# Kernel optimization log

Measured on AMD Instinct MI355X. Metric: run time of the kernel, lower is better.

## Reference

```python
import jax, jax.numpy as jnp
import numpy as np

C, FF, NH = 128, 2048, 8
B, D, H, W = 1, 16, 16, 16
EPS = 1e-5

def setup_inputs() -> dict:
    key = jax.random.key(0)
    ks = jax.random.split(key, 20)
    s = 0.02
    inp = {
        'x': jax.random.normal(ks[0], (B, C, D, H, W), jnp.float32),
        'Wq': jax.random.normal(ks[1], (C, C), jnp.float32) * s,
        'bq': jnp.zeros((C,), jnp.float32),
        'Wk': jax.random.normal(ks[2], (C, C), jnp.float32) * s,
        'bk': jnp.zeros((C,), jnp.float32),
        'Wv': jax.random.normal(ks[3], (C, C), jnp.float32) * s,
        'bv': jnp.zeros((C,), jnp.float32),
        'Wo': jax.random.normal(ks[4], (C, C), jnp.float32) * s,
        'bo': jnp.zeros((C,), jnp.float32),
        'W1': jax.random.normal(ks[5], (FF, C), jnp.float32) * s,
        'b1': jnp.zeros((FF,), jnp.float32),
        'W2': jax.random.normal(ks[6], (C, FF), jnp.float32) * s,
        'b2': jnp.zeros((C,), jnp.float32),
        'g1': jnp.ones((C,), jnp.float32),
        'be1': jnp.zeros((C,), jnp.float32),
        'g2': jnp.ones((C,), jnp.float32),
        'be2': jnp.zeros((C,), jnp.float32),
    }
    return inp

def _layernorm(t, g, b):
    # normalize over last (channel) dim, biased variance like torch LayerNorm
    m = jnp.mean(t, axis=-1, keepdims=True)
    v = jnp.mean(jnp.square(t - m), axis=-1, keepdims=True)
    return (t - m) * jax.lax.rsqrt(v + EPS) * g + b

def reference(x, Wq, bq, Wk, bk, Wv, bv, Wo, bo, W1, b1, W2, b2, g1, be1, g2, be2):
    b_, c, d, h, w = x.shape
    n = d * h * w
    hd = c // NH
    xf = x.reshape(b_, c, n)  # [B,C,N]
    # 1x1 conv3d == per-voxel linear over channels
    q = jnp.einsum('oc,bcn->bon', Wq, xf) + bq[:, None]
    k = jnp.einsum('oc,bcn->bon', Wk, xf) + bk[:, None]
    v = jnp.einsum('oc,bcn->bon', Wv, xf) + bv[:, None]
    q = q.reshape(b_, NH, hd, n)
    k = k.reshape(b_, NH, hd, n)
    v = v.reshape(b_, NH, hd, n)
    scores = jnp.einsum('bhcd,bhce->bhde', q, k) / (hd ** 0.5)  # [B,NH,N,N]
    probs = jax.nn.softmax(scores, axis=-1)
    attn = jnp.einsum('bhde,bhce->bhcd', probs, v).reshape(b_, c, n)
    attn = jnp.einsum('oc,bcn->bon', Wo, attn) + bo[:, None]
    x1 = xf + attn  # residual (dropout = identity at eval)
    x1 = _layernorm(x1.transpose(0, 2, 1), g1, be1)  # [B,N,C]
    hmid = jax.nn.relu(jnp.einsum('fc,bnc->bnf', W1, x1) + b1)
    ffn = jnp.einsum('cf,bnf->bnc', W2, hmid) + b2
    x2 = _layernorm(x1 + ffn, g2, be2)
    return x2.transpose(0, 2, 1).reshape(b_, c, d, h, w)
```

## Files before the change

### kernel.cpp

```cpp
#include <hip/hip_runtime.h>
#include <hip/hip_bf16.h>

typedef __hip_bfloat16 bf16;
typedef short short8 __attribute__((ext_vector_type(8)));
typedef float f32x4 __attribute__((ext_vector_type(4)));

#define C_   128
#define N_   4096
#define NH_  8
#define HD_  16
#define FF_  2048
#define SCALE_Q 0.360673760222241f

__device__ __forceinline__ unsigned short f2bf_bits(float f) {
    bf16 h = __float2bfloat16(f);
    return *reinterpret_cast<unsigned short*>(&h);
}
__device__ __forceinline__ unsigned int pack_trunc(float lo, float hi) {
    return (__float_as_uint(hi) & 0xffff0000u) | (__float_as_uint(lo) >> 16);
}
__device__ __forceinline__ short f2bf_trunc(float f) {
    return (short)(__float_as_uint(f) >> 16);
}
__device__ __forceinline__ float bfs2f(short s) {
    return __uint_as_float(((unsigned int)(unsigned short)s) << 16);
}
__device__ __forceinline__ float fast_exp2(float x) {
    return __builtin_amdgcn_exp2f(x);
}
__device__ __forceinline__ f32x4 mfma16(short8 a, short8 b, f32x4 c) {
    return __builtin_amdgcn_mfma_f32_16x16x32_bf16(a, b, c, 0, 0, 0);
}
__device__ __forceinline__ int kpos(int ko) { return ((ko & 15) << 1) + (ko >> 4); }

__global__ void k_prep(const float* __restrict__ Wq, const float* __restrict__ Wk,
                       const float* __restrict__ Wv, const float* __restrict__ Wo,
                       const float* __restrict__ W1, const float* __restrict__ W2,
                       const float* __restrict__ x,
                       bf16* __restrict__ Wqkvf, bf16* __restrict__ Wof,
                       bf16* __restrict__ W1f, bf16* __restrict__ W2f,
                       bf16* __restrict__ xTf)
{
    const int i = blockIdx.x * 256 + threadIdx.x;
    if (i < 49152) {
        const int o = i >> 7, k = i & 127;
        const float v = (o < 128) ? Wq[i] : (o < 256) ? Wk[i - 16384] : Wv[i - 32768];
        const int pk = kpos(k & 31);
        Wqkvf[(((o >> 4) << 2) + (k >> 5)) * 512 + (((pk >> 3) << 4) + (o & 15)) * 8 + (pk & 7)]
            = __float2bfloat16(v);
    } else if (i < 65536) {
        const int j = i - 49152, o = j >> 7, k = j & 127;
        const int pk = kpos(k & 31);
        Wof[(((o >> 4) << 2) + (k >> 5)) * 512 + (((pk >> 3) << 4) + (o & 15)) * 8 + (pk & 7)]
            = __float2bfloat16(Wo[j]);
    } else if (i < 327680) {
        const int j = i - 65536, o = j >> 7, k = j & 127;
        const int pk = kpos(k & 31);
        W1f[(((o >> 4) << 2) + (k >> 5)) * 512 + (((pk >> 3) << 4) + (o & 15)) * 8 + (pk & 7)]
            = __float2bfloat16(W1[j]);
    } else if (i < 589824) {
        const int j = i - 327680, o = j >> 11, k = j & 2047;
        const int pk = kpos(k & 31);
        W2f[(((o >> 4) << 6) + (k >> 5)) * 512 + (((pk >> 3) << 4) + (o & 15)) * 8 + (pk & 7)]
            = __float2bfloat16(W2[j]);
    } else if (i < 1114112) {
        const int j = i - 589824, c = j >> 12, n = j & 4095;
        const int pk = kpos(c & 31);
        xTf[(((n >> 4) << 2) + (c >> 5)) * 512 + (((pk >> 3) << 4) + (n & 15)) * 8 + (pk & 7)]
            = __float2bfloat16(x[j]);
    }
}

__global__ void __launch_bounds__(256) k_qkv(
    const bf16* __restrict__ xTf, const bf16* __restrict__ Wqkvf,
    const float* __restrict__ bq, const float* __restrict__ bk, const float* __restrict__ bv,
    bf16* __restrict__ qf, bf16* __restrict__ kf, bf16* __restrict__ vf)
{
    const int tid = threadIdx.x, wave = tid >> 6, lane = tid & 63;
    const int col = lane & 15, quad = lane >> 4;
    const int gw = blockIdx.x * 4 + wave;
    const int rt = gw / 24, ct = gw % 24;
    f32x4 acc = {};
    #pragma unroll
    for (int c = 0; c < 4; ++c) {
        short8 a = *(const short8*)(xTf + ((size_t)(rt * 4 + c) << 9) + lane * 8);
        short8 b = *(const short8*)(Wqkvf + ((size_t)(ct * 4 + c) << 9) + lane * 8);
        acc = mfma16(a, b, acc);
    }
    #pragma unroll
    for (int r = 0; r < 4; ++r) {
        const int m = rt * 16 + quad * 4 + r;
        const int n = ct * 16 + col;
        const float v = acc[r];
        if (n < 128) {
            const int h = n >> 4, ch = n & 15;
            qf[((h << 8) + (m >> 4)) * 256 + (((ch >> 3) << 4) + (m & 15)) * 8 + (ch & 7)] =
                __float2bfloat16((v + bq[n]) * SCALE_Q);
        } else if (n < 256) {
            const int c2 = n - 128, h = c2 >> 4, ch = c2 & 15;
            kf[((h << 8) + (m >> 4)) * 256 + (((ch >> 3) << 4) + (m & 15)) * 8 + (ch & 7)] =
                __float2bfloat16(v + bk[c2]);
        } else {
            const int c2 = n - 256, h = c2 >> 4, ch = c2 & 15;
            const int ko = m & 31;
            const int pos = ((ko & 15) << 1) + (ko >> 4);
            vf[((h << 7) + (m >> 5)) * 512 + (((pos >> 3) << 4) + ch) * 8 + (pos & 7)] =
                __float2bfloat16(v + bv[c2]);
        }
    }
}

__global__ void __launch_bounds__(256)
attn_kernel(const bf16* __restrict__ qf, const bf16* __restrict__ kf,
            const bf16* __restrict__ vf, bf16* __restrict__ af)
{
    __shared__ __align__(16) union {
        unsigned int P[4][2][320];
        float comb[4][64][8];
    } sh;
    const int tid = threadIdx.x, wave = tid >> 6, lane = tid & 63;
    const int col = lane & 15, quad = lane >> 4;
    const int gw = blockIdx.x;
    const int h  = gw >> 8;
    const int tile = gw & 255;
    const f32x4 zero = {};

    short8 aq = {};
    if (quad < 2)
        aq = *(const short8*)(qf + ((size_t)((h << 8) + tile) << 8) + lane * 8);

    f32x4 accO0 = {}, accO1 = {};
    float L[4] = {0.f, 0.f, 0.f, 0.f};

    const int kbeg = wave << 10;
    unsigned int* P0 = &sh.P[wave][0][0];
    unsigned int* P1 = &sh.P[wave][1][0];

    for (int i = 0; i < 32; i += 2) {
        const int mA = kbeg + (i << 5);
        const int mB = mA + 32;

        short8 bkA0 = {}, bkA1 = {}, bkB0 = {}, bkB1 = {};
        if (quad < 2) {
            const bf16* ka = kf + ((size_t)((h << 8) + (mA >> 4)) << 8) + lane * 8;
            bkA0 = *(const short8*)(ka);
            bkA1 = *(const short8*)(ka + 256);
            bkB0 = *(const short8*)(ka + 512);
            bkB1 = *(const short8*)(ka + 768);
        }
        f32x4 s0 = mfma16(aq, bkA0, zero);
        f32x4 s1 = mfma16(aq, bkA1, zero);
        f32x4 s2 = mfma16(aq, bkB0, zero);
        f32x4 s3 = mfma16(aq, bkB1, zero);
        #pragma unroll
        for (int r = 0; r < 4; ++r) {
            const float p0 = fast_exp2(s0[r]);
            const float p1 = fast_exp2(s1[r]);
            const float p2 = fast_exp2(s2[r]);
            const float p3 = fast_exp2(s3[r]);
            L[r] += (p0 + p1) + (p2 + p3);
            P0[(quad * 4 + r) * 20 + col] = pack_trunc(p0, p1);
            P1[(quad * 4 + r) * 20 + col] = pack_trunc(p2, p3);
        }
        short8 vA = *(const short8*)(vf + ((size_t)((h << 7) + (mA >> 5)) << 9) + lane * 8);
        short8 vB = *(const short8*)(vf + ((size_t)((h << 7) + (mB >> 5)) << 9) + lane * 8);
        short8 ap0 = *(const short8*)((const short*)P0 + col * 40 + quad * 8);
        accO0 = mfma16(ap0, vA, accO0);
        short8 ap1 = *(const short8*)((const short*)P1 + col * 40 + quad * 8);
        accO1 = mfma16(ap1, vB, accO1);
    }

    f32x4 accO;
    #pragma unroll
    for (int r = 0; r < 4; ++r) accO[r] = accO0[r] + accO1[r];

    __syncthreads();
    #pragma unroll
    for (int r = 0; r < 4; ++r) {
        sh.comb[wave][lane][r]     = accO[r];
        sh.comb[wave][lane][4 + r] = L[r];
    }
    __syncthreads();

    if (wave == 0) {
        #pragma unroll
        for (int r = 0; r < 4; ++r) {
            float O = sh.comb[0][lane][r] + sh.comb[1][lane][r]
                    + sh.comb[2][lane][r] + sh.comb[3][lane][r];
            float l = sh.comb[0][lane][4+r] + sh.comb[1][lane][4+r]
                    + sh.comb[2][lane][4+r] + sh.comb[3][lane][4+r];
            l += __shfl_xor(l, 1); l += __shfl_xor(l, 2);
            l += __shfl_xor(l, 4); l += __shfl_xor(l, 8);
            const int row16 = quad * 4 + r;
            const int pk = (col << 1) + (h & 1);
            af[((tile << 2) + (h >> 1)) * 512 + (((pk >> 3) << 4) + row16) * 8 + (pk & 7)] =
                __float2bfloat16(O / l);
        }
    }
}

__global__ void __launch_bounds__(256, 1)
k_mega(const bf16* __restrict__ af, const bf16* __restrict__ xTf,
       const bf16* __restrict__ Wof, const bf16* __restrict__ W1f, const bf16* __restrict__ W2f,
       const float* __restrict__ bo, const float* __restrict__ b1, const float* __restrict__ b2,
       const float* __restrict__ g1, const float* __restrict__ be1,
       const float* __restrict__ g2, const float* __restrict__ be2,
       float* __restrict__ out)
{
    __shared__ __align__(16) unsigned int Pb[4][2][320];
    __shared__ float comb[96][64];
    const int tid = threadIdx.x, wave = tid >> 6, lane = tid & 63;
    const int col = lane & 15, quad = lane >> 4;
    const int rt = blockIdx.x, n0 = rt << 4;
    const f32x4 zero = {};

    short8 ao[4], xt[4];
    #pragma unroll
    for (int c = 0; c < 4; ++c) {
        ao[c] = *(const short8*)(af  + ((size_t)(rt * 4 + c) << 9) + lane * 8);
        xt[c] = *(const short8*)(xTf + ((size_t)(rt * 4 + c) << 9) + lane * 8);
    }
    f32x4 d[8];
    #pragma unroll
    for (int t = 0; t < 8; ++t) d[t] = zero;
    #pragma unroll
    for (int t = 0; t < 8; ++t)
        #pragma unroll
        for (int c = 0; c < 4; ++c) {
            short8 b = *(const short8*)(Wof + ((size_t)(t * 4 + c) << 9) + lane * 8);
            d[t] = mfma16(ao[c], b, d[t]);
        }
    #pragma unroll
    for (int t = 0; t < 8; ++t) {
        const float bt = bo[t * 16 + col];
        #pragma unroll
        for (int r = 0; r < 4; ++r) d[t][r] += bt;
    }

    float x1f[4][8];
    #pragma unroll
    for (int c = 0; c < 4; ++c) {
        unsigned int* Pw = &Pb[wave][c & 1][0];
        const short* Ps = (const short*)Pw;
        #pragma unroll
        for (int r = 0; r < 4; ++r)
            Pw[(quad * 4 + r) * 20 + col] = pack_trunc(d[2 * c][r], d[2 * c + 1][r]);
        short8 ar = *(const short8*)(Ps + col * 40 + quad * 8);
        #pragma unroll
        for (int j = 0; j < 8; ++j)
            x1f[c][j] = bfs2f(ar[j]) + bfs2f(xt[c][j]);
    }

    float s = 0.f, ss = 0.f;
    #pragma unroll
    for (int c = 0; c < 4; ++c)
        #pragma unroll
        for (int j = 0; j < 8; ++j) { s += x1f[c][j]; ss += x1f[c][j] * x1f[c][j]; }
    s  += __shfl_xor(s, 16);  s  += __shfl_xor(s, 32);
    ss += __shfl_xor(ss, 16); ss += __shfl_xor(ss, 32);
    const float m1 = s * (1.f / 128.f);
    const float rstd1 = rsqrtf(ss * (1.f / 128.f) - m1 * m1 + 1e-5f);
    short8 aq1[4];
    #pragma unroll
    for (int c = 0; c < 4; ++c)
        #pragma unroll
        for (int j = 0; j < 8; ++j) {
            const int pos = quad * 8 + j;
            const int ko = ((pos & 1) << 4) + (pos >> 1);
            const int ch = c * 32 + ko;
            aq1[c][j] = f2bf_trunc((x1f[c][j] - m1) * rstd1 * g1[ch] + be1[ch]);
        }

    f32x4 ACC[8];
    #pragma unroll
    for (int t = 0; t < 8; ++t) ACC[t] = zero;
    for (int i = 0; i < 16; ++i) {
        const int ffc = (wave << 4) + i;
        f32x4 p0 = zero, p1 = zero;
        #pragma unroll
        for (int c = 0; c < 4; ++c) {
            short8 b = *(const short8*)(W1f + ((size_t)(ffc * 8 + c) << 9) + lane * 8);
            p0 = mfma16(aq1[c], b, p0);
        }
        #pragma unroll
        for (int c = 0; c < 4; ++c) {
            short8 b = *(const short8*)(W1f + ((size_t)(ffc * 8 + 4 + c) << 9) + lane * 8);
            p1 = mfma16(aq1[c], b, p1);
        }
        const float bb0 = b1[ffc * 32 + col], bb1 = b1[ffc * 32 + 16 + col];
        unsigned int* Pw = &Pb[wave][i & 1][0];
        #pragma unroll
        for (int r = 0; r < 4; ++r)
            Pw[(quad * 4 + r) * 20 + col] =
                pack_trunc(fmaxf(p0[r] + bb0, 0.f), fmaxf(p1[r] + bb1, 0.f));
        short8 ah = *(const short8*)((const short*)Pw + col * 40 + quad * 8);
        #pragma unroll
        for (int t = 0; t < 8; ++t) {
            short8 bw = *(const short8*)(W2f + ((size_t)(t * 64 + ffc) << 9) + lane * 8);
            ACC[t] = mfma16(ah, bw, ACC[t]);
        }
    }

    if (wave) {
        #pragma unroll
        for (int t = 0; t < 8; ++t)
            #pragma unroll
            for (int r = 0; r < 4; ++r)
                comb[(wave - 1) * 32 + t * 4 + r][lane] = ACC[t][r];
    }
    __syncthreads();
    if (wave == 0) {
        #pragma unroll
        for (int t = 0; t < 8; ++t)
            #pragma unroll
            for (int r = 0; r < 4; ++r)
                ACC[t][r] += comb[t * 4 + r][lane] + comb[32 + t * 4 + r][lane]
                           + comb[64 + t * 4 + r][lane];
        short* xb = (short*)&Pb[0][0][0];
        #pragma unroll
        for (int c = 0; c < 4; ++c)
            *(short8*)(xb + (col * 4 + c) * 32 + quad * 8) = aq1[c];
        float t2[8][4];
        #pragma unroll
        for (int t = 0; t < 8; ++t) {
            const int ch = t * 16 + col;
            const int pk = (col << 1) + (t & 1);
            const int c = t >> 1;
            const float bb = b2[ch];
            #pragma unroll
            for (int r = 0; r < 4; ++r)
                t2[t][r] = ACC[t][r] + bb + bfs2f(xb[((quad * 4 + r) * 4 + c) * 32 + pk]);
        }
        #pragma unroll
        for (int r = 0; r < 4; ++r) {
            float S = 0.f, SS = 0.f;
            #pragma unroll
            for (int t = 0; t < 8; ++t) { S += t2[t][r]; SS += t2[t][r] * t2[t][r]; }
            S  += __shfl_xor(S, 1);  S  += __shfl_xor(S, 2);
            S  += __shfl_xor(S, 4);  S  += __shfl_xor(S, 8);
            SS += __shfl_xor(SS, 1); SS += __shfl_xor(SS, 2);
            SS += __shfl_xor(SS, 4); SS += __shfl_xor(SS, 8);
            const float m2 = S * (1.f / 128.f);
            const float rstd2 = rsqrtf(SS * (1.f / 128.f) - m2 * m2 + 1e-5f);
            #pragma unroll
            for (int t = 0; t < 8; ++t) {
                const int ch = t * 16 + col;
                out[(size_t)ch * N_ + n0 + quad * 4 + r] =
                    (t2[t][r] - m2) * rstd2 * g2[ch] + be2[ch];
            }
        }
    }
}

extern "C" void kernel_launch(void* const* d_in, const int* in_sizes, int n_in,
                              void* d_out, int out_size, void* d_ws, size_t ws_size,
                              hipStream_t stream) {
    const float* x   = (const float*)d_in[0];
    const float* Wq  = (const float*)d_in[1];
    const float* bq  = (const float*)d_in[2];
    const float* Wk  = (const float*)d_in[3];
    const float* bk  = (const float*)d_in[4];
    const float* Wv  = (const float*)d_in[5];
    const float* bv  = (const float*)d_in[6];
    const float* Wo  = (const float*)d_in[7];
    const float* bo  = (const float*)d_in[8];
    const float* W1  = (const float*)d_in[9];
    const float* b1  = (const float*)d_in[10];
    const float* W2  = (const float*)d_in[11];
    const float* b2  = (const float*)d_in[12];
    const float* g1  = (const float*)d_in[13];
    const float* be1 = (const float*)d_in[14];
    const float* g2  = (const float*)d_in[15];
    const float* be2 = (const float*)d_in[16];
    float* out = (float*)d_out;

    char* ws = (char*)d_ws;
    bf16* xTf   = (bf16*)(ws + 0);
    bf16* qf    = (bf16*)(ws + 1048576);
    bf16* kf    = (bf16*)(ws + 2097152);
    bf16* vf    = (bf16*)(ws + 3145728);
    bf16* af    = (bf16*)(ws + 4194304);
    bf16* Wqkvf = (bf16*)(ws + 5242880);
    bf16* Wof   = (bf16*)(ws + 5341184);
    bf16* W1f   = (bf16*)(ws + 5373952);
    bf16* W2f   = (bf16*)(ws + 5898240);

    k_prep<<<4352, 256, 0, stream>>>(Wq, Wk, Wv, Wo, W1, W2, x, Wqkvf, Wof, W1f, W2f, xTf);
    k_qkv<<<1536, 256, 0, stream>>>(xTf, Wqkvf, bq, bk, bv, qf, kf, vf);
    attn_kernel<<<2048, 256, 0, stream>>>(qf, kf, vf, af);
    k_mega<<<256, 256, 0, stream>>>(af, xTf, Wof, W1f, W2f, bo, b1, b2,
                                    g1, be1, g2, be2, out);
}
```

Measured before the change: 143.4 us.

## Vectorize prep and QKV stores via per-wave tiles and shared-memory staging

k_prep becomes one wave per 512-element packed MFMA block. It reads float4 rows and writes one short8 per lane, and the x transpose is staged through shared memory, replacing scattered 2-byte stores. k_qkv stages its 16x16 output tile in LDS and writes it back with coalesced 16-byte stores. The QKV rounding changes from round-to-nearest to truncation. In the attention kernel the packed 32-bit P stores are split into 16-bit stores with a new column layout. The aim is fewer memory transactions in the prep and projection kernels, at the cost of extra LDS traffic and a small precision change.

```diff
diff --git a/kernel.cpp b/kernel.cpp
--- a/kernel.cpp
+++ b/kernel.cpp
@@ -31,43 +31,59 @@
 __device__ __forceinline__ f32x4 mfma16(short8 a, short8 b, f32x4 c) {
     return __builtin_amdgcn_mfma_f32_16x16x32_bf16(a, b, c, 0, 0, 0);
 }
-__device__ __forceinline__ int kpos(int ko) { return ((ko & 15) << 1) + (ko >> 4); }
-
-__global__ void k_prep(const float* __restrict__ Wq, const float* __restrict__ Wk,
-                       const float* __restrict__ Wv, const float* __restrict__ Wo,
-                       const float* __restrict__ W1, const float* __restrict__ W2,
-                       const float* __restrict__ x,
-                       bf16* __restrict__ Wqkvf, bf16* __restrict__ Wof,
-                       bf16* __restrict__ W1f, bf16* __restrict__ W2f,
-                       bf16* __restrict__ xTf)
+
+__global__ void __launch_bounds__(256) k_prep(
+    const float* __restrict__ Wq, const float* __restrict__ Wk,
+    const float* __restrict__ Wv, const float* __restrict__ Wo,
+    const float* __restrict__ W1, const float* __restrict__ W2,
+    const float* __restrict__ x,
+    bf16* __restrict__ Wqkvf, bf16* __restrict__ Wof,
+    bf16* __restrict__ W1f, bf16* __restrict__ W2f,
+    bf16* __restrict__ xTf)
 {
-    const int i = blockIdx.x * 256 + threadIdx.x;
-    if (i < 49152) {
-        const int o = i >> 7, k = i & 127;
-        const float v = (o < 128) ? Wq[i] : (o < 256) ? Wk[i - 16384] : Wv[i - 32768];
-        const int pk = kpos(k & 31);
-        Wqkvf[(((o >> 4) << 2) + (k >> 5)) * 512 + (((pk >> 3) << 4) + (o & 15)) * 8 + (pk & 7)]
-            = __float2bfloat16(v);
-    } else if (i < 65536) {
-        const int j = i - 49152, o = j >> 7, k = j & 127;
-        const int pk = kpos(k & 31);
-        Wof[(((o >> 4) << 2) + (k >> 5)) * 512 + (((pk >> 3) << 4) + (o & 15)) * 8 + (pk & 7)]
-            = __float2bfloat16(Wo[j]);
-    } else if (i < 327680) {
-        const int j = i - 65536, o = j >> 7, k = j & 127;
-        const int pk = kpos(k & 31);
-        W1f[(((o >> 4) << 2) + (k >> 5)) * 512 + (((pk >> 3) << 4) + (o & 15)) * 8 + (pk & 7)]
-            = __float2bfloat16(W1[j]);
-    } else if (i < 589824) {
-        const int j = i - 327680, o = j >> 11, k = j & 2047;
-        const int pk = kpos(k & 31);
-        W2f[(((o >> 4) << 6) + (k >> 5)) * 512 + (((pk >> 3) << 4) + (o & 15)) * 8 + (pk & 7)]
-            = __float2bfloat16(W2[j]);
-    } else if (i < 1114112) {
-        const int j = i - 589824, c = j >> 12, n = j & 4095;
-        const int pk = kpos(c & 31);
-        xTf[(((n >> 4) << 2) + (c >> 5)) * 512 + (((pk >> 3) << 4) + (n & 15)) * 8 + (pk & 7)]
-            = __float2bfloat16(x[j]);
+    __shared__ float xs[4][512];
+    const int tid = threadIdx.x, wave = tid >> 6, lane = tid & 63;
+    const int gw = blockIdx.x * 4 + wave;
+    const int q = lane >> 4;
+
+    if (gw < 1152) {
+        const float* src; bf16* dst; int K, otile, kch, blk;
+        if (gw < 96)        { src = 0;  dst = Wqkvf; K = 128;  otile = gw >> 2;          kch = gw & 3;  blk = gw; }
+        else if (gw < 128)  { int i = gw - 96;  src = Wo; dst = Wof;  K = 128;  otile = i >> 2; kch = i & 3;  blk = i; }
+        else if (gw < 640)  { int i = gw - 128; src = W1; dst = W1f;  K = 128;  otile = i >> 2; kch = i & 3;  blk = i; }
+        else                { int i = gw - 640; src = W2; dst = W2f;  K = 2048; otile = i >> 6; kch = i & 63; blk = i; }
+        const int o = otile * 16 + (lane & 15);
+        const int k0 = kch * 32 + 4 * q;
+        const float* row;
+        if (gw < 96) {
+            row = (o < 128) ? (Wq + o * 128) : (o < 256) ? (Wk + (o - 128) * 128)
+                                             : (Wv + (o - 256) * 128);
+        } else {
+            row = src + (size_t)o * K;
+        }
+        const float4 A = *(const float4*)(row + k0);
+        const float4 B = *(const float4*)(row + k0 + 16);
+        short8 v;
+        v[0] = f2bf_bits(A.x); v[1] = f2bf_bits(B.x);
+        v[2] = f2bf_bits(A.y); v[3] = f2bf_bits(B.y);
+        v[4] = f2bf_bits(A.z); v[5] = f2bf_bits(B.z);
+        v[6] = f2bf_bits(A.w); v[7] = f2bf_bits(B.w);
+        *(short8*)((short*)dst + (size_t)blk * 512 + lane * 8) = v;
+    } else {
+        const int i = gw - 1152;
+        const int n0 = (i >> 2) << 4, c0 = (i & 3) << 5;
+        float* S = xs[wave];
+        const int cl = lane & 31, ns = (lane >> 5) << 3;
+        const float* p = x + (size_t)(c0 + cl) * N_ + n0 + ns;
+        *(float4*)(S + cl * 16 + ns)     = *(const float4*)(p);
+        *(float4*)(S + cl * 16 + ns + 4) = *(const float4*)(p + 4);
+        short8 v;
+        #pragma unroll
+        for (int j = 0; j < 8; ++j) {
+            const int ko = ((j & 1) << 4) + 4 * q + (j >> 1);
+            v[j] = f2bf_bits(S[ko * 16 + (lane & 15)]);
+        }
+        *(short8*)((short*)xTf + (size_t)i * 512 + lane * 8) = v;
     }
 }
 
@@ -76,6 +92,7 @@
     const float* __restrict__ bq, const float* __restrict__ bk, const float* __restrict__ bv,
     bf16* __restrict__ qf, bf16* __restrict__ kf, bf16* __restrict__ vf)
 {
+    __shared__ short tb[4][512];
     const int tid = threadIdx.x, wave = tid >> 6, lane = tid & 63;
     const int col = lane & 15, quad = lane >> 4;
     const int gw = blockIdx.x * 4 + wave;
@@ -87,26 +104,34 @@
         short8 b = *(const short8*)(Wqkvf + ((size_t)(ct * 4 + c) << 9) + lane * 8);
         acc = mfma16(a, b, acc);
     }
-    #pragma unroll
-    for (int r = 0; r < 4; ++r) {
-        const int m = rt * 16 + quad * 4 + r;
-        const int n = ct * 16 + col;
-        const float v = acc[r];
-        if (n < 128) {
-            const int h = n >> 4, ch = n & 15;
-            qf[((h << 8) + (m >> 4)) * 256 + (((ch >> 3) << 4) + (m & 15)) * 8 + (ch & 7)] =
-                __float2bfloat16((v + bq[n]) * SCALE_Q);
-        } else if (n < 256) {
-            const int c2 = n - 128, h = c2 >> 4, ch = c2 & 15;
-            kf[((h << 8) + (m >> 4)) * 256 + (((ch >> 3) << 4) + (m & 15)) * 8 + (ch & 7)] =
-                __float2bfloat16(v + bk[c2]);
-        } else {
-            const int c2 = n - 256, h = c2 >> 4, ch = c2 & 15;
-            const int ko = m & 31;
-            const int pos = ((ko & 15) << 1) + (ko >> 4);
-            vf[((h << 7) + (m >> 5)) * 512 + (((pos >> 3) << 4) + ch) * 8 + (pos & 7)] =
-                __float2bfloat16(v + bv[c2]);
-        }
+    short* T = tb[wave];
+    if (ct < 8) {
+        const float bb = bq[ct * 16 + col];
+        #pragma unroll
+        for (int r = 0; r < 4; ++r)
+            T[(col >> 3) * 128 + (quad * 4 + r) * 8 + (col & 7)] =
+                f2bf_trunc((acc[r] + bb) * SCALE_Q);
+    } else if (ct < 16) {
+        const float bb = bk[(ct - 8) * 16 + col];
+        #pragma unroll
+        for (int r = 0; r < 4; ++r)
+            T[(col >> 3) * 128 + (quad * 4 + r) * 8 + (col & 7)] =
+                f2bf_trunc(acc[r] + bb);
+    } else {
+        const float bb = bv[(ct - 16) * 16 + col];
+        #pragma unroll
+        for (int r = 0; r < 4; ++r) {
+            const int ko = quad * 4 + r;
+            T[(ko >> 3) * 128 + col * 8 + (ko & 7)] = f2bf_trunc(acc[r] + bb);
+        }
+    }
+    if (lane < 32) {
+        short8 w = *(const short8*)(T + lane * 8);
+        short* dst;
+        if (ct < 8)       dst = (short*)qf + ((ct << 8) + rt) * 256;
+        else if (ct < 16) dst = (short*)kf + (((ct - 8) << 8) + rt) * 256;
+        else              dst = (short*)vf + ((((ct - 16) << 7) + (rt >> 1)) << 9) + (rt & 1) * 256;
+        *(short8*)(dst + lane * 8) = w;
     }
 }
 
@@ -133,8 +158,8 @@
     float L[4] = {0.f, 0.f, 0.f, 0.f};
 
     const int kbeg = wave << 10;
-    unsigned int* P0 = &sh.P[wave][0][0];
-    unsigned int* P1 = &sh.P[wave][1][0];
+    short* P0 = (short*)&sh.P[wave][0][0];
+    short* P1 = (short*)&sh.P[wave][1][0];
 
     for (int i = 0; i < 32; i += 2) {
         const int mA = kbeg + (i << 5);
@@ -159,14 +184,17 @@
             const float p2 = fast_exp2(s2[r]);
             const float p3 = fast_exp2(s3[r]);
             L[r] += (p0 + p1) + (p2 + p3);
-            P0[(quad * 4 + r) * 20 + col] = pack_trunc(p0, p1);
-            P1[(quad * 4 + r) * 20 + col] = pack_trunc(p2, p3);
+            const int row = (quad * 4 + r) * 40;
+            P0[row + col]      = f2bf_trunc(p0);
+            P0[row + 16 + col] = f2bf_trunc(p1);
+            P1[row + col]      = f2bf_trunc(p2);
+            P1[row + 16 + col] = f2bf_trunc(p3);
         }
         short8 vA = *(const short8*)(vf + ((size_t)((h << 7) + (mA >> 5)) << 9) + lane * 8);
         short8 vB = *(const short8*)(vf + ((size_t)((h << 7) + (mB >> 5)) << 9) + lane * 8);
-        short8 ap0 = *(const short8*)((const short*)P0 + col * 40 + quad * 8);
+        short8 ap0 = *(const short8*)(P0 + col * 40 + quad * 8);
         accO0 = mfma16(ap0, vA, accO0);
-        short8 ap1 = *(const short8*)((const short*)P1 + col * 40 + quad * 8);
+        short8 ap1 = *(const short8*)(P1 + col * 40 + quad * 8);
         accO1 = mfma16(ap1, vB, accO1);
     }
 
@@ -385,7 +413,7 @@
     bf16* W1f   = (bf16*)(ws + 5373952);
     bf16* W2f   = (bf16*)(ws + 5898240);
 
-    k_prep<<<4352, 256, 0, stream>>>(Wq, Wk, Wv, Wo, W1, W2, x, Wqkvf, Wof, W1f, W2f, xTf);
+    k_prep<<<544, 256, 0, stream>>>(Wq, Wk, Wv, Wo, W1, W2, x, Wqkvf, Wof, W1f, W2f, xTf);
     k_qkv<<<1536, 256, 0, stream>>>(xTf, Wqkvf, bq, bk, bv, qf, kf, vf);
     attn_kernel<<<2048, 256, 0, stream>>>(qf, kf, vf, af);
     k_mega<<<256, 256, 0, stream>>>(af, xTf, Wof, W1f, W2f, bo, b1, b2,
```

New measurement: 143.7 us. About the same (+0.2%).
